# Performance work log

Hardware: AMD Instinct MI355X
Metric: run time of the kernel (lower is better)

## Reference

```python
import jax, jax.numpy as jnp
import numpy as np

K_LAYERS = 2   # top-k layers kept in zeta routing
K_EXPERTS = 2  # top-k experts kept in alpha routing


def _topk_sparse_softmax(logits, k):
    """Keep top-k along last axis, set rest to -inf, softmax. logits [..., N]."""
    lead = logits.shape[:-1]
    n = logits.shape[-1]
    flat = logits.reshape(-1, n)
    vals, idx = jax.lax.top_k(flat, k)                      # [R,k]
    sparse = jnp.full_like(flat, -jnp.inf)
    rows = jnp.arange(flat.shape[0])[:, None]
    sparse = sparse.at[rows, idx].set(vals)
    return jax.nn.softmax(sparse, axis=-1).reshape(*lead, n)


def _lora_layer(h, W, b, A, B, zeta_l, alpha_l):
    """One backbone Linear + gated LoRA expert mixture + ReLU.
    h [B,in], W [out,in], A [E,r,in], B [E,out,r], zeta_l [B], alpha_l [B,E].
    """
    lin = h @ W.T + b                                       # [B,out]
    t = jnp.einsum('bi,eri->ber', h, A)                     # [B,E,r]
    tw = t * alpha_l[:, :, None]                            # weight experts early
    lora_sum = jnp.einsum('ber,eor->bo', tw, B)             # [B,out]
    return jax.nn.relu(lin + zeta_l[:, None] * lora_sum)


def _routing(domain_ids, dom_emb, layer_pos, Wi1, bi1, Wi2, bi2,
             Wa1, ba1, Wa2, ba2, gate_logits, R_benefit):
    M, H = dom_emb.shape
    L = layer_pos.shape[0]
    router_inp = jnp.concatenate([
        jnp.broadcast_to(dom_emb[:, None, :], (M, L, H)),
        jnp.broadcast_to(layer_pos[None, :, :], (M, L, H)),
    ], axis=-1)                                             # [M,L,2H]
    hz = jax.nn.relu(router_inp @ Wi1.T + bi1)
    zeta_logits = (hz @ Wi2.T + bi2)[..., 0]                # [M,L]
    zeta_all = _topk_sparse_softmax(zeta_logits, K_LAYERS)
    ha = jax.nn.relu(router_inp @ Wa1.T + ba1)
    alpha_logits = ha @ Wa2.T + ba2                         # [M,L,E]
    alpha_all = _topk_sparse_softmax(alpha_logits, K_EXPERTS)
    # gated benefit matrix, row-normalized
    R = jax.nn.softplus(gate_logits) * R_benefit
    R = R / jnp.clip(R.sum(-1, keepdims=True), 1e-12)
    zeta_agg = R @ zeta_all                                 # [M,L]
    alpha_agg = jnp.einsum('mn,nle->mle', R, alpha_all)     # [M,L,E]
    return zeta_agg[domain_ids], alpha_agg[domain_ids]      # [B,L],[B,L,E]


def setup_inputs() -> dict:
    key = jax.random.key(0)
    ks = jax.random.split(key, 32)
    Bsz, D0, D1, D2, D3 = 16384, 2048, 2048, 1024, 512
    E, r, M, H, L = 4, 8, 8, 64, 3
    s = 0.02
    return {
        'x': jax.random.normal(ks[0], (Bsz, D0), jnp.float32),
        'domain_ids': jax.random.randint(ks[1], (Bsz,), 0, M),
        'W1': jax.random.normal(ks[2], (D1, D0)) * s, 'b1': jnp.zeros((D1,)),
        'W2': jax.random.normal(ks[3], (D2, D1)) * s, 'b2': jnp.zeros((D2,)),
        'W3': jax.random.normal(ks[4], (D3, D2)) * s, 'b3': jnp.zeros((D3,)),
        'A1': jax.random.normal(ks[5], (E, r, D0)) * s, 'B1': jax.random.normal(ks[6], (E, D1, r)) * s,
        'A2': jax.random.normal(ks[7], (E, r, D1)) * s, 'B2': jax.random.normal(ks[8], (E, D2, r)) * s,
        'A3': jax.random.normal(ks[9], (E, r, D2)) * s, 'B3': jax.random.normal(ks[10], (E, D3, r)) * s,
        'dom_emb': jax.random.normal(ks[11], (M, H)) * s,
        'layer_pos': jax.random.normal(ks[12], (L, H)) * s,
        'Wi1': jax.random.normal(ks[13], (H, 2 * H)) * 0.1, 'bi1': jnp.zeros((H,)),
        'Wi2': jax.random.normal(ks[14], (1, H)) * 0.1, 'bi2': jnp.zeros((1,)),
        'Wa1': jax.random.normal(ks[15], (H, 2 * H)) * 0.1, 'ba1': jnp.zeros((H,)),
        'Wa2': jax.random.normal(ks[16], (E, H)) * 0.1, 'ba2': jnp.zeros((E,)),
        'gate_logits': jax.random.normal(ks[17], (M, M)) * 0.1,
        'R_benefit': jax.random.uniform(ks[18], (M, M)),
    }


def reference(x, domain_ids, W1, b1, W2, b2, W3, b3,
              A1, B1, A2, B2, A3, B3,
              dom_emb, layer_pos, Wi1, bi1, Wi2, bi2,
              Wa1, ba1, Wa2, ba2, gate_logits, R_benefit):
    zeta, alpha = _routing(domain_ids, dom_emb, layer_pos, Wi1, bi1, Wi2, bi2,
                           Wa1, ba1, Wa2, ba2, gate_logits, R_benefit)
    h = _lora_layer(x, W1, b1, A1, B1, zeta[:, 0], alpha[:, 0])
    h = _lora_layer(h, W2, b2, A2, B2, zeta[:, 1], alpha[:, 1])
    h = _lora_layer(h, W3, b3, A3, B3, zeta[:, 2], alpha[:, 2])
    return h
```

## Files before the change

kernel.cpp:

```cpp
#include <hip/hip_runtime.h>

typedef __bf16 bf16_t;
typedef __bf16 bf16x8 __attribute__((ext_vector_type(8)));
typedef __bf16 bf16x4_v __attribute__((ext_vector_type(4)));
typedef float f32x4 __attribute__((ext_vector_type(4)));

#define AS1 __attribute__((address_space(1)))
#define AS3 __attribute__((address_space(3)))

__device__ __forceinline__ void gload_lds16(const void* g, void* l) {
    __builtin_amdgcn_global_load_lds((AS1 void*)(void*)g, (AS3 void*)l, 16, 0, 0);
}

__global__ void routing_kernel(
    const float* __restrict__ dom_emb, const float* __restrict__ layer_pos,
    const float* __restrict__ Wi1, const float* __restrict__ bi1,
    const float* __restrict__ Wi2, const float* __restrict__ bi2,
    const float* __restrict__ Wa1, const float* __restrict__ ba1,
    const float* __restrict__ Wa2, const float* __restrict__ ba2,
    const float* __restrict__ gate_logits, const float* __restrict__ R_benefit,
    float* __restrict__ salpha)
{
    constexpr int M = 8, L = 3, E = 4, H = 64;
    __shared__ float zl[M * L];
    __shared__ float al[M * L][E];
    __shared__ float zeta_all[M][L];
    __shared__ float alpha_all[M][L][E];
    const int t = threadIdx.x;
    const int ml = t >> 3, js = t & 7;
    if (ml < M * L) {
        const int m = ml / L, l = ml % L;
        float zacc = 0.f;
        float aacc[E] = {0.f, 0.f, 0.f, 0.f};
        for (int jj = 0; jj < 8; ++jj) {
            const int j = js * 8 + jj;
            float hz = bi1[j], ha = ba1[j];
            for (int i = 0; i < H; ++i) {
                const float de = dom_emb[m * H + i];
                const float lp = layer_pos[l * H + i];
                hz += de * Wi1[j * 2 * H + i] + lp * Wi1[j * 2 * H + H + i];
                ha += de * Wa1[j * 2 * H + i] + lp * Wa1[j * 2 * H + H + i];
            }
            hz = fmaxf(hz, 0.f); ha = fmaxf(ha, 0.f);
            zacc += hz * Wi2[j];
            for (int e = 0; e < E; ++e) aacc[e] += ha * Wa2[e * H + j];
        }
        #pragma unroll
        for (int off = 4; off >= 1; off >>= 1) {
            zacc += __shfl_down(zacc, off, 8);
            for (int e = 0; e < E; ++e) aacc[e] += __shfl_down(aacc[e], off, 8);
        }
        if (js == 0) {
            zl[ml] = zacc + bi2[0];
            for (int e = 0; e < E; ++e) al[ml][e] = aacc[e] + ba2[e];
        }
    }
    __syncthreads();
    if (t < M) {
        const int m = t;
        float v[3] = { zl[m * L + 0], zl[m * L + 1], zl[m * L + 2] };
        int di = 0; float dv = v[0];
        for (int i = 1; i < 3; ++i) if (v[i] <= dv) { dv = v[i]; di = i; }
        float mx = -1e30f;
        for (int i = 0; i < 3; ++i) if (i != di) mx = fmaxf(mx, v[i]);
        float s = 0.f, ev[3];
        for (int i = 0; i < 3; ++i) { ev[i] = (i == di) ? 0.f : expf(v[i] - mx); s += ev[i]; }
        for (int i = 0; i < 3; ++i) zeta_all[m][i] = ev[i] / s;
        for (int l = 0; l < L; ++l) {
            float a[4];
            for (int e = 0; e < 4; ++e) a[e] = al[m * L + l][e];
            int i1 = 0;
            for (int e = 1; e < 4; ++e) if (a[e] > a[i1]) i1 = e;
            int i2 = -1;
            for (int e = 0; e < 4; ++e) { if (e == i1) continue; if (i2 < 0 || a[e] > a[i2]) i2 = e; }
            const float mx2 = fmaxf(a[i1], a[i2]);
            const float e1 = expf(a[i1] - mx2), e2 = expf(a[i2] - mx2);
            const float ss = e1 + e2;
            for (int e = 0; e < 4; ++e) alpha_all[m][l][e] = 0.f;
            alpha_all[m][l][i1] = e1 / ss;
            alpha_all[m][l][i2] = e2 / ss;
        }
    }
    __syncthreads();
    if (t < M) {
        const int m = t;
        float Rrow[8]; float rs = 0.f;
        for (int n = 0; n < M; ++n) {
            const float g = gate_logits[m * M + n];
            const float rr = log1pf(expf(g)) * R_benefit[m * M + n];
            Rrow[n] = rr; rs += rr;
        }
        rs = fmaxf(rs, 1e-12f);
        for (int l = 0; l < L; ++l) {
            float zag = 0.f, aag[4] = {0.f, 0.f, 0.f, 0.f};
            for (int n = 0; n < M; ++n) {
                const float w = Rrow[n] / rs;
                zag += w * zeta_all[n][l];
                for (int e = 0; e < 4; ++e) aag[e] += w * alpha_all[n][l][e];
            }
            for (int e = 0; e < 4; ++e) salpha[(m * L + l) * 4 + e] = zag * aag[e];
        }
    }
}

__global__ void cvt_fused(const float* __restrict__ s0, const float* __restrict__ s1,
                          const float* __restrict__ s2, const float* __restrict__ s3,
                          const float* __restrict__ s4, const float* __restrict__ s5,
                          bf16_t* __restrict__ dst)
{
    const int i = blockIdx.x * 256 + threadIdx.x;
    constexpr int b0 = 1048576;
    constexpr int b1 = b0 + 524288;
    constexpr int b2 = b1 + 131072;
    constexpr int b3 = b2 + 16384;
    constexpr int b4 = b3 + 16384;
    constexpr int b5 = b4 + 8192;
    if (i >= b5) return;
    const float* src; int rel;
    if (i < b0)      { src = s0; rel = i; }
    else if (i < b1) { src = s1; rel = i - b0; }
    else if (i < b2) { src = s2; rel = i - b1; }
    else if (i < b3) { src = s3; rel = i - b2; }
    else if (i < b4) { src = s4; rel = i - b3; }
    else             { src = s5; rel = i - b4; }
    const float4 v = ((const float4*)src)[rel];
    bf16x4_v o;
    o[0] = (__bf16)v.x; o[1] = (__bf16)v.y; o[2] = (__bf16)v.z; o[3] = (__bf16)v.w;
    ((bf16x4_v*)dst)[i] = o;
}

__global__ void bepi_fused(const float* __restrict__ B1, const float* __restrict__ B2,
                           const float* __restrict__ B3, bf16_t* __restrict__ dst)
{
    const int idx = blockIdx.x * 256 + threadIdx.x;
    constexpr int c1 = 2048 * 32, c2 = c1 + 1024 * 32, c3 = c2 + 512 * 32;
    if (idx >= c3) return;
    const float* B; int rel, Dout;
    if (idx < c1)      { B = B1; rel = idx;      Dout = 2048; }
    else if (idx < c2) { B = B2; rel = idx - c1; Dout = 1024; }
    else               { B = B3; rel = idx - c2; Dout = 512; }
    const int o = rel >> 5, c = rel & 31, e = c >> 3, r = c & 7;
    dst[idx] = (__bf16)B[((size_t)e * Dout + o) * 8 + r];
}

template<bool F32IN>
__global__ void __launch_bounds__(256) tw_kernel(
    const void* __restrict__ hin, bf16_t* __restrict__ xb_out,
    const bf16_t* __restrict__ Acat, const float* __restrict__ salpha,
    const int* __restrict__ dom, const int layer, const int K,
    bf16_t* __restrict__ TWb)
{
    const int t = threadIdx.x, wid = t >> 6, lane = t & 63;
    const int rb = blockIdx.x * 64 + wid * 16;
    const int ln15 = lane & 15, kg = (lane >> 4) * 8;
    const int row = rb + ln15;
    f32x4 acc0 = {0.f, 0.f, 0.f, 0.f}, acc1 = {0.f, 0.f, 0.f, 0.f};
    const bf16_t* pa0 = Acat + (size_t)ln15 * K + kg;
    const bf16_t* pa1 = pa0 + (size_t)16 * K;
    for (int k0 = 0; k0 < K; k0 += 32) {
        bf16x8 a;
        if constexpr (F32IN) {
            const float* px = (const float*)hin + (size_t)row * K + k0 + kg;
            const float4 x0 = *(const float4*)px;
            const float4 x1 = *(const float4*)(px + 4);
            a[0] = (__bf16)x0.x; a[1] = (__bf16)x0.y; a[2] = (__bf16)x0.z; a[3] = (__bf16)x0.w;
            a[4] = (__bf16)x1.x; a[5] = (__bf16)x1.y; a[6] = (__bf16)x1.z; a[7] = (__bf16)x1.w;
            *(bf16x8*)(xb_out + (size_t)row * K + k0 + kg) = a;
        } else {
            a = *(const bf16x8*)((const bf16_t*)hin + (size_t)row * K + k0 + kg);
        }
        const bf16x8 b0 = *(const bf16x8*)(pa0 + k0);
        const bf16x8 b1 = *(const bf16x8*)(pa1 + k0);
        acc0 = __builtin_amdgcn_mfma_f32_16x16x32_bf16(a, b0, acc0, 0, 0, 0);
        acc1 = __builtin_amdgcn_mfma_f32_16x16x32_bf16(a, b1, acc1, 0, 0, 0);
    }
    const int rbase = rb + (lane >> 4) * 4;
    #pragma unroll
    for (int i = 0; i < 4; ++i) {
        const int r2 = rbase + i;
        const int d = dom[r2];
        const float* sa = salpha + (d * 3 + layer) * 4;
        const float s0 = sa[ln15 >> 3];
        const float s1 = sa[2 + (ln15 >> 3)];
        TWb[(size_t)r2 * 32 + ln15]      = (__bf16)(acc0[i] * s0);
        TWb[(size_t)r2 * 32 + 16 + ln15] = (__bf16)(acc1[i] * s1);
    }
}


__device__ __forceinline__ void stage_chunk32(const bf16_t* g, char* chunk, int t) {
    const int row = t >> 2;
    const int sl = t & 3;
    const int src = sl ^ (((row >> 3) & 1) << 1);
    gload_lds16(g + (size_t)row * 32 + src * 8, chunk + t * 16);
}

template<int K>
__global__ void __launch_bounds__(512, 2) gemm_lora8(
    const bf16_t* __restrict__ Abuf, const bf16_t* __restrict__ Wbuf,
    const float* __restrict__ bias, const bf16_t* __restrict__ TWb,
    const bf16_t* __restrict__ Bepi, bf16_t* __restrict__ outp,
    const int N, const int nwg_n)
{
    __shared__ __align__(1024) char lds[131072];
    const int t = threadIdx.x;
    const int wid = t >> 6, lane = t & 63;
    const int wm = wid >> 2, wn = wid & 3, wnh = wn >> 1;
    const int cpx = gridDim.x >> 3;
    const int wg = (blockIdx.x & 7) * cpx + (blockIdx.x >> 3);
    const int row0 = (wg / nwg_n) * 256, col0 = (wg % nwg_n) * 256;

    const int r15 = lane & 15;
    const int swb = ((lane >> 4) ^ (((lane >> 3) & 1) << 1)) << 4;

    const char* aBase = lds + (wm << 14) + (r15 << 6) + swb;
    const char* bBase = lds + 65536 + (wnh << 14) + ((wn & 1) << 12) + (r15 << 6) + swb;
    char* const dBase = lds + t * 16;

    const int srow = t >> 2, ssl = t & 3;
    const int ssrc = ssl ^ (((srow >> 3) & 1) << 1);
    const bf16_t* sA = Abuf + (size_t)(row0 + srow) * K + ssrc * 8;
    const bf16_t* sB = Wbuf + (size_t)(col0 + srow) * K + ssrc * 8;
    constexpr size_t halfA = (size_t)128 * K;

    f32x4 acc[8][4] = {};
    bf16x8 aF[4], bF[4];

    #define RD_A(P, KQ, MB) do { _Pragma("unroll") for (int i_ = 0; i_ < 4; ++i_) \
        aF[i_] = *(const bf16x8*)(aBase + (P)*32768 + (KQ)*8192 + ((MB)+i_)*1024); } while (0)
    #define RD_B(P, KQ) do { _Pragma("unroll") for (int n_ = 0; n_ < 4; ++n_) \
        bF[n_] = *(const bf16x8*)(bBase + (P)*32768 + (KQ)*8192 + n_*1024); } while (0)

    auto mfma16 = [&](int mbase) {
        __builtin_amdgcn_s_setprio(1);
        #pragma unroll
        for (int mf = 0; mf < 4; ++mf)
            #pragma unroll
            for (int nf = 0; nf < 4; ++nf)
                acc[mbase + mf][nf] =
                    __builtin_amdgcn_mfma_f32_16x16x32_bf16(aF[mf], bF[nf], acc[mbase + mf][nf], 0, 0, 0);
        __builtin_amdgcn_s_setprio(0);
    };
    #define BAR() __builtin_amdgcn_s_barrier()

    constexpr int NT = K >> 6;

    gload_lds16(sA,              dBase + 0);
    gload_lds16(sA + halfA,      dBase + 16384);
    gload_lds16(sB,              dBase + 65536);
    gload_lds16(sB + halfA,      dBase + 65536 + 16384);
    gload_lds16(sA + 32,         dBase + 8192);
    gload_lds16(sA + halfA + 32, dBase + 24576);
    gload_lds16(sB + 32,         dBase + 65536 + 8192);
    gload_lds16(sB + halfA + 32, dBase + 65536 + 24576);
    asm volatile("s_waitcnt vmcnt(4)" ::: "memory");
    __builtin_amdgcn_s_barrier();

    const bf16_t* pA0 = sA + 64;
    const bf16_t* pA1 = sA + halfA + 64;
    const bf16_t* pB0 = sB + 64;
    const bf16_t* pB1 = sB + halfA + 64;

    #define TILE(P, MORE, TOFF) do {                                            \
                                           \
        RD_A(P, 0, 0);                                                           \
        RD_B(P, 0);                                                              \
        if (MORE) { gload_lds16(pA0 + (TOFF), dBase + ((P)^1)*32768 + 0);        \
                    gload_lds16(pA1 + (TOFF), dBase + ((P)^1)*32768 + 16384); }  \
        BAR();                                                                   \
        mfma16(0);                                                               \
        BAR();                                                                   \
                  \
        RD_A(P, 0, 4);                                                           \
        if (MORE) {                                                              \
            gload_lds16(pB0 + (TOFF), dBase + 65536 + ((P)^1)*32768 + 0);        \
            gload_lds16(pB1 + (TOFF), dBase + 65536 + ((P)^1)*32768 + 16384);    \
            asm volatile("s_waitcnt vmcnt(4)" ::: "memory");                     \
        } else {                                                                 \
            asm volatile("s_waitcnt vmcnt(0)" ::: "memory");                     \
        }                                                                        \
        BAR();                                                                   \
        mfma16(4);                                                               \
        BAR();                                                                   \
                                           \
        RD_A(P, 1, 4);                                                           \
        RD_B(P, 1);                                                              \
        if (MORE) { gload_lds16(pA0 + (TOFF) + 32, dBase + ((P)^1)*32768 + 8192);  \
                    gload_lds16(pA1 + (TOFF) + 32, dBase + ((P)^1)*32768 + 24576);} \
        BAR();                                                                   \
        mfma16(4);                                                               \
        BAR();                                                                   \
                \
        RD_A(P, 1, 0);                                                           \
        if (MORE) {                                                              \
            gload_lds16(pB0 + (TOFF) + 32, dBase + 65536 + ((P)^1)*32768 + 8192);  \
            gload_lds16(pB1 + (TOFF) + 32, dBase + 65536 + ((P)^1)*32768 + 24576); \
            asm volatile("s_waitcnt vmcnt(4)" ::: "memory");                     \
        }                                                                        \
        BAR();                                                                   \
        mfma16(0);                                                               \
        BAR();                                                                   \
    } while (0)

    #pragma unroll 1
    for (int T = 0; T < NT - 2; T += 2) {
        TILE(0, true, 0);
        TILE(1, true, 64);
        pA0 += 128; pA1 += 128; pB0 += 128; pB1 += 128;
    }
    TILE(0, true, 0);
    TILE(1, false, 64);

    {
        stage_chunk32(TWb + (size_t)row0 * 32,          lds + 0,             t);
        stage_chunk32(TWb + (size_t)(row0 + 128) * 32,  lds + 16384,         t);
        stage_chunk32(Bepi + (size_t)col0 * 32,         lds + 65536,         t);
        stage_chunk32(Bepi + (size_t)(col0 + 128) * 32, lds + 65536 + 16384, t);
        asm volatile("s_waitcnt vmcnt(0)" ::: "memory");
        __builtin_amdgcn_s_barrier();
        RD_B(0, 0);
        RD_A(0, 0, 0);
        mfma16(0);
        RD_A(0, 0, 4);
        mfma16(4);
    }

    const int orow = row0 + wm * 128 + (lane >> 4) * 4;
    const int ocol = col0 + wn * 64 + r15;
    #pragma unroll
    for (int nf = 0; nf < 4; ++nf) {
        const int col = ocol + nf * 16;
        const float bn = bias[col];
        #pragma unroll
        for (int mf = 0; mf < 8; ++mf) {
            const int rbase = orow + mf * 16;
            #pragma unroll
            for (int i = 0; i < 4; ++i) {
                const float v = fmaxf(acc[mf][nf][i] + bn, 0.f);
                outp[(size_t)(rbase + i) * N + col] = (__bf16)v;
            }
        }
    }
    #undef TILE
    #undef RD_A
    #undef RD_B
    #undef BAR
}

#define BM 128
#define BN 128
#define BK 32

template<bool OUT_F32, int K>
__global__ void __launch_bounds__(256) gemm_lora(
    const bf16_t* __restrict__ Abuf, const bf16_t* __restrict__ Wbuf,
    const float* __restrict__ bias, const bf16_t* __restrict__ TWb,
    const bf16_t* __restrict__ Bepi, void* __restrict__ outp,
    const int N)
{
    __shared__ bf16_t lA[BM * BK];
    __shared__ bf16_t lB[BN * BK];
    const int t = threadIdx.x;
    const int row0 = blockIdx.y * BM;
    const int col0 = blockIdx.x * BN;
    const int wid = t >> 6, lane = t & 63;
    const int wr = wid >> 1, wc = wid & 1;
    const int ln15 = lane & 15, kg = (lane >> 4) * 8;
    const int srow = t >> 2, sg8 = (t & 3) * 8;
    const bf16_t* gA = Abuf + (size_t)(row0 + srow) * K + sg8;
    const bf16_t* gB = Wbuf + (size_t)(col0 + srow) * K + sg8;
    bf16_t* ldA  = &lA[t * 8];
    bf16_t* ldA2 = &lA[2048 + t * 8];
    bf16_t* ldB  = &lB[t * 8];
    bf16_t* ldB2 = &lB[2048 + t * 8];
    f32x4 acc[4][4] = {};
    const int aoff = (wr * 64 + ln15) * BK + kg;
    const int boff = (wc * 64 + ln15) * BK + kg;

    auto compute_tile = [&]() {
        bf16x8 af[4], bfr[4];
        #pragma unroll
        for (int m = 0; m < 4; ++m) af[m] = *(const bf16x8*)&lA[aoff + m * 16 * BK];
        #pragma unroll
        for (int n = 0; n < 4; ++n) bfr[n] = *(const bf16x8*)&lB[boff + n * 16 * BK];
        #pragma unroll
        for (int m = 0; m < 4; ++m)
            #pragma unroll
            for (int n = 0; n < 4; ++n)
                acc[m][n] = __builtin_amdgcn_mfma_f32_16x16x32_bf16(af[m], bfr[n], acc[m][n], 0, 0, 0);
    };

    constexpr size_t half = (size_t)64 * K;
    constexpr int nk = K / BK;
    #pragma unroll 1
    for (int kt = 0; kt < nk; ++kt) {
        gload_lds16(gA + kt * BK, ldA);
        gload_lds16(gA + half + kt * BK, ldA2);
        gload_lds16(gB + kt * BK, ldB);
        gload_lds16(gB + half + kt * BK, ldB2);
        __syncthreads();
        compute_tile();
        __syncthreads();
    }
    gload_lds16(TWb + (size_t)(row0 + srow) * 32 + sg8, ldA);
    gload_lds16(TWb + (size_t)(row0 + 64 + srow) * 32 + sg8, ldA2);
    gload_lds16(Bepi + (size_t)(col0 + srow) * 32 + sg8, ldB);
    gload_lds16(Bepi + (size_t)(col0 + 64 + srow) * 32 + sg8, ldB2);
    __syncthreads();
    compute_tile();

    const int orow = row0 + wr * 64 + (lane >> 4) * 4;
    const int ocol = col0 + wc * 64 + ln15;
    #pragma unroll
    for (int n = 0; n < 4; ++n) {
        const int col = ocol + n * 16;
        const float bn = bias[col];
        #pragma unroll
        for (int m = 0; m < 4; ++m) {
            const int rbase = orow + m * 16;
            #pragma unroll
            for (int i = 0; i < 4; ++i) {
                const float v = fmaxf(acc[m][n][i] + bn, 0.f);
                if constexpr (OUT_F32)
                    ((float*)outp)[(size_t)(rbase + i) * N + col] = v;
                else
                    ((bf16_t*)outp)[(size_t)(rbase + i) * N + col] = (__bf16)v;
            }
        }
    }
}

extern "C" void kernel_launch(void* const* d_in, const int* in_sizes, int n_in,
                              void* d_out, int out_size, void* d_ws, size_t ws_size,
                              hipStream_t stream)
{
    const float* x    = (const float*)d_in[0];
    const int*   dom  = (const int*)d_in[1];
    const float* W1   = (const float*)d_in[2];  const float* b1  = (const float*)d_in[3];
    const float* W2   = (const float*)d_in[4];  const float* b2  = (const float*)d_in[5];
    const float* W3   = (const float*)d_in[6];  const float* b3  = (const float*)d_in[7];
    const float* A1   = (const float*)d_in[8];  const float* B1  = (const float*)d_in[9];
    const float* A2   = (const float*)d_in[10]; const float* B2  = (const float*)d_in[11];
    const float* A3   = (const float*)d_in[12]; const float* B3  = (const float*)d_in[13];
    const float* dome = (const float*)d_in[14]; const float* lpos = (const float*)d_in[15];
    const float* Wi1  = (const float*)d_in[16]; const float* bi1 = (const float*)d_in[17];
    const float* Wi2  = (const float*)d_in[18]; const float* bi2 = (const float*)d_in[19];
    const float* Wa1  = (const float*)d_in[20]; const float* ba1 = (const float*)d_in[21];
    const float* Wa2  = (const float*)d_in[22]; const float* ba2 = (const float*)d_in[23];
    const float* gate = (const float*)d_in[24]; const float* Rb  = (const float*)d_in[25];
    (void)in_sizes; (void)n_in; (void)out_size; (void)ws_size;

    constexpr int Bsz = 16384, D0 = 2048, D1 = 2048, D2 = 1024, D3 = 512;

    char* ws = (char*)d_ws;
    size_t off = 0;
    auto alloc = [&](size_t bytes) -> void* {
        void* p = ws + off;
        off = (off + bytes + 255) & ~(size_t)255;
        return p;
    };
    float*  salpha = (float*) alloc(8 * 3 * 4 * sizeof(float));
    bf16_t* W1b = (bf16_t*)alloc((size_t)D1 * D0 * 2);
    bf16_t* W2b = (bf16_t*)alloc((size_t)D2 * D1 * 2);
    bf16_t* W3b = (bf16_t*)alloc((size_t)D3 * D2 * 2);
    bf16_t* Ac1 = (bf16_t*)alloc((size_t)32 * D0 * 2);
    bf16_t* Ac2 = (bf16_t*)alloc((size_t)32 * D1 * 2);
    bf16_t* Ac3 = (bf16_t*)alloc((size_t)32 * D2 * 2);
    bf16_t* Be1 = (bf16_t*)alloc((size_t)D1 * 32 * 2);
    bf16_t* Be2 = (bf16_t*)alloc((size_t)D2 * 32 * 2);
    bf16_t* Be3 = (bf16_t*)alloc((size_t)D3 * 32 * 2);
    bf16_t* TWb = (bf16_t*)alloc((size_t)Bsz * 32 * 2);
    bf16_t* xb  = (bf16_t*)alloc((size_t)Bsz * D0 * 2);
    bf16_t* h1b = (bf16_t*)alloc((size_t)Bsz * D1 * 2);
    bf16_t* h2b = xb;

    routing_kernel<<<1, 256, 0, stream>>>(dome, lpos, Wi1, bi1, Wi2, bi2,
                                          Wa1, ba1, Wa2, ba2, gate, Rb, salpha);

    cvt_fused<<<6816, 256, 0, stream>>>(W1, W2, W3, A1, A2, A3, W1b);
    bepi_fused<<<448, 256, 0, stream>>>(B1, B2, B3, Be1);

    tw_kernel<true><<<Bsz / 64, 256, 0, stream>>>(x, xb, Ac1, salpha, dom, 0, D0, TWb);
    gemm_lora8<2048><<<(Bsz / 256) * (D1 / 256), 512, 0, stream>>>(xb, W1b, b1, TWb, Be1, h1b, D1, D1 / 256);
    tw_kernel<false><<<Bsz / 64, 256, 0, stream>>>(h1b, nullptr, Ac2, salpha, dom, 1, D1, TWb);
    gemm_lora8<2048><<<(Bsz / 256) * (D2 / 256), 512, 0, stream>>>(h1b, W2b, b2, TWb, Be2, h2b, D2, D2 / 256);
    tw_kernel<false><<<Bsz / 64, 256, 0, stream>>>(h2b, nullptr, Ac3, salpha, dom, 2, D2, TWb);
    gemm_lora<true, 1024><<<dim3(D3 / BN, Bsz / BM), 256, 0, stream>>>(h2b, W3b, b3, TWb, Be3, d_out, D3);
}
```

Measured before the change: 405.8 us.

## Split tw_kernel K loop into two accumulator chains and drop post-MFMA barriers

The tw_kernel K reduction is split into two halves with independent accumulators, so each iteration issues twice as many loads and four MFMAs, giving more memory-level and instruction-level parallelism. The main GEMM tile macro drops the barrier after each MFMA group, leaving one barrier per phase, and adds a single barrier before the epilogue restages LDS. Removing the barriers risks LDS races if a wave's register reads from a buffer are not finished before another wave's global_load_lds overwrites it. Correctness depends on the register reads having completed before the next phase's barrier.

```diff
diff --git a/kernel.cpp b/kernel.cpp
--- a/kernel.cpp
+++ b/kernel.cpp
@@ -154,26 +154,40 @@
     const int rb = blockIdx.x * 64 + wid * 16;
     const int ln15 = lane & 15, kg = (lane >> 4) * 8;
     const int row = rb + ln15;
-    f32x4 acc0 = {0.f, 0.f, 0.f, 0.f}, acc1 = {0.f, 0.f, 0.f, 0.f};
+    const int Kh = K >> 1;
+    f32x4 a0l = {0.f,0.f,0.f,0.f}, a1l = {0.f,0.f,0.f,0.f};
+    f32x4 a0h = {0.f,0.f,0.f,0.f}, a1h = {0.f,0.f,0.f,0.f};
     const bf16_t* pa0 = Acat + (size_t)ln15 * K + kg;
     const bf16_t* pa1 = pa0 + (size_t)16 * K;
-    for (int k0 = 0; k0 < K; k0 += 32) {
-        bf16x8 a;
+    for (int k0 = 0; k0 < Kh; k0 += 32) {
+        bf16x8 al, ah;
         if constexpr (F32IN) {
             const float* px = (const float*)hin + (size_t)row * K + k0 + kg;
             const float4 x0 = *(const float4*)px;
             const float4 x1 = *(const float4*)(px + 4);
-            a[0] = (__bf16)x0.x; a[1] = (__bf16)x0.y; a[2] = (__bf16)x0.z; a[3] = (__bf16)x0.w;
-            a[4] = (__bf16)x1.x; a[5] = (__bf16)x1.y; a[6] = (__bf16)x1.z; a[7] = (__bf16)x1.w;
-            *(bf16x8*)(xb_out + (size_t)row * K + k0 + kg) = a;
+            const float4 y0 = *(const float4*)(px + Kh);
+            const float4 y1 = *(const float4*)(px + Kh + 4);
+            al[0] = (__bf16)x0.x; al[1] = (__bf16)x0.y; al[2] = (__bf16)x0.z; al[3] = (__bf16)x0.w;
+            al[4] = (__bf16)x1.x; al[5] = (__bf16)x1.y; al[6] = (__bf16)x1.z; al[7] = (__bf16)x1.w;
+            ah[0] = (__bf16)y0.x; ah[1] = (__bf16)y0.y; ah[2] = (__bf16)y0.z; ah[3] = (__bf16)y0.w;
+            ah[4] = (__bf16)y1.x; ah[5] = (__bf16)y1.y; ah[6] = (__bf16)y1.z; ah[7] = (__bf16)y1.w;
+            *(bf16x8*)(xb_out + (size_t)row * K + k0 + kg) = al;
+            *(bf16x8*)(xb_out + (size_t)row * K + Kh + k0 + kg) = ah;
         } else {
-            a = *(const bf16x8*)((const bf16_t*)hin + (size_t)row * K + k0 + kg);
-        }
-        const bf16x8 b0 = *(const bf16x8*)(pa0 + k0);
-        const bf16x8 b1 = *(const bf16x8*)(pa1 + k0);
-        acc0 = __builtin_amdgcn_mfma_f32_16x16x32_bf16(a, b0, acc0, 0, 0, 0);
-        acc1 = __builtin_amdgcn_mfma_f32_16x16x32_bf16(a, b1, acc1, 0, 0, 0);
-    }
+            al = *(const bf16x8*)((const bf16_t*)hin + (size_t)row * K + k0 + kg);
+            ah = *(const bf16x8*)((const bf16_t*)hin + (size_t)row * K + Kh + k0 + kg);
+        }
+        const bf16x8 b0l = *(const bf16x8*)(pa0 + k0);
+        const bf16x8 b1l = *(const bf16x8*)(pa1 + k0);
+        const bf16x8 b0h = *(const bf16x8*)(pa0 + Kh + k0);
+        const bf16x8 b1h = *(const bf16x8*)(pa1 + Kh + k0);
+        a0l = __builtin_amdgcn_mfma_f32_16x16x32_bf16(al, b0l, a0l, 0, 0, 0);
+        a1l = __builtin_amdgcn_mfma_f32_16x16x32_bf16(al, b1l, a1l, 0, 0, 0);
+        a0h = __builtin_amdgcn_mfma_f32_16x16x32_bf16(ah, b0h, a0h, 0, 0, 0);
+        a1h = __builtin_amdgcn_mfma_f32_16x16x32_bf16(ah, b1h, a1h, 0, 0, 0);
+    }
+    const f32x4 acc0 = a0l + a0h;
+    const f32x4 acc1 = a1l + a1h;
     const int rbase = rb + (lane >> 4) * 4;
     #pragma unroll
     for (int i = 0; i < 4; ++i) {
@@ -269,7 +283,6 @@
                     gload_lds16(pA1 + (TOFF), dBase + ((P)^1)*32768 + 16384); }  \
         BAR();                                                                   \
         mfma16(0);                                                               \
-        BAR();                                                                   \
                   \
         RD_A(P, 0, 4);                                                           \
         if (MORE) {                                                              \
@@ -281,7 +294,6 @@
         }                                                                        \
         BAR();                                                                   \
         mfma16(4);                                                               \
-        BAR();                                                                   \
                                            \
         RD_A(P, 1, 4);                                                           \
         RD_B(P, 1);                                                              \
@@ -289,7 +301,6 @@
                     gload_lds16(pA1 + (TOFF) + 32, dBase + ((P)^1)*32768 + 24576);} \
         BAR();                                                                   \
         mfma16(4);                                                               \
-        BAR();                                                                   \
                 \
         RD_A(P, 1, 0);                                                           \
         if (MORE) {                                                              \
@@ -299,7 +310,6 @@
         }                                                                        \
         BAR();                                                                   \
         mfma16(0);                                                               \
-        BAR();                                                                   \
     } while (0)
 
     #pragma unroll 1
@@ -312,6 +322,7 @@
     TILE(1, false, 64);
 
     {
+        __builtin_amdgcn_s_barrier();
         stage_chunk32(TWb + (size_t)row0 * 32,          lds + 0,             t);
         stage_chunk32(TWb + (size_t)(row0 + 128) * 32,  lds + 16384,         t);
         stage_chunk32(Bepi + (size_t)col0 * 32,         lds + 65536,         t);
```

After: 393.0 us. 3.2% less time.
